# Kernel optimization log

Hardware: AMD Instinct MI355X
Metric: run time of the kernel (lower is better)

## Reference

```python
import jax, jax.numpy as jnp
import numpy as np

HIDDEN = 2048
NHEADS = 16
NKV = 4
HEAD_DIM = 128
B, T = 2, 2048


def setup_inputs() -> dict:
    key = jax.random.key(0)
    ks = jax.random.split(key, 7)
    x = jax.random.normal(ks[0], (B, T, HIDDEN), dtype=jnp.float32)
    # rope tables [T, head_dim//2]
    inv_freq = 1.0 / (10000.0 ** (jnp.arange(0, HEAD_DIM // 2, dtype=jnp.float32) / (HEAD_DIM // 2)))
    pos = jnp.arange(T, dtype=jnp.float32)
    ang = pos[:, None] * inv_freq[None, :]
    cos, sin = jnp.cos(ang), jnp.sin(ang)
    s = 0.02
    wq = jax.random.normal(ks[1], (HIDDEN, NHEADS * HEAD_DIM), dtype=jnp.float32) * s
    wk = jax.random.normal(ks[2], (HIDDEN, NKV * HEAD_DIM), dtype=jnp.float32) * s
    wv = jax.random.normal(ks[3], (HIDDEN, NKV * HEAD_DIM), dtype=jnp.float32) * s
    wo = jax.random.normal(ks[4], (NHEADS * HEAD_DIM, HIDDEN), dtype=jnp.float32) * s
    return {"x": x, "cos": cos, "sin": sin, "wq": wq, "wk": wk, "wv": wv, "wo": wo}


def _apply_rope(x, cos, sin):
    # x: [B, H, T, D]; cos/sin: [T, D//2]
    hd = x.shape[-1]
    x1, x2 = x[..., : hd // 2], x[..., hd // 2 :]
    c = cos[None, None, : x.shape[2], :]
    s = sin[None, None, : x.shape[2], :]
    return jnp.concatenate([x1 * c - x2 * s, x2 * c + x1 * s], axis=-1)


def reference(x, cos, sin, wq, wk, wv, wo):
    Bb, Tt, _ = x.shape
    q = (x @ wq).reshape(Bb, Tt, NHEADS, HEAD_DIM).transpose(0, 2, 1, 3)  # [B,H,T,D]
    k = (x @ wk).reshape(Bb, Tt, NKV, HEAD_DIM).transpose(0, 2, 1, 3)    # [B,Hk,T,D]
    v = (x @ wv).reshape(Bb, Tt, NKV, HEAD_DIM).transpose(0, 2, 1, 3)
    q = _apply_rope(q, cos, sin)
    k = _apply_rope(k, cos, sin)
    groups = NHEADS // NKV
    k = jnp.repeat(k, groups, axis=1)  # [B,H,T,D]
    v = jnp.repeat(v, groups, axis=1)
    scale = 1.0 / jnp.sqrt(jnp.asarray(HEAD_DIM, dtype=x.dtype))
    scores = jnp.einsum("bhqd,bhkd->bhqk", q, k) * scale
    causal = jnp.tril(jnp.ones((Tt, Tt), dtype=bool))
    scores = jnp.where(causal[None, None, :, :], scores, jnp.asarray(-jnp.inf, dtype=scores.dtype))
    attn = jax.nn.softmax(scores, axis=-1)
    out = jnp.einsum("bhqk,bhkd->bhqd", attn, v)
    out = out.transpose(0, 2, 1, 3).reshape(Bb, Tt, NHEADS * HEAD_DIM)
    return out @ wo
```

## Files before the change

kernel.cpp:

```cpp
#include <hip/hip_runtime.h>

#define HIDDEN 2048
#define NHEADS 16
#define NKV 4
#define HEAD_DIM 128
#define BB 2
#define TT 2048
#define MROWS (BB * TT)
#define NQKV (NHEADS * HEAD_DIM + 2 * NKV * HEAD_DIM)

typedef __attribute__((ext_vector_type(8))) short short8;
typedef __attribute__((ext_vector_type(4))) float f32x4;

#if __has_builtin(__builtin_amdgcn_exp2f)
#define EXP2F __builtin_amdgcn_exp2f
#else
#define EXP2F exp2f
#endif

__device__ __forceinline__ unsigned short f2bf(float f) {
    unsigned int u = __float_as_uint(f);
    unsigned int r = u + 0x7fffu + ((u >> 16) & 1u);
    return (unsigned short)(r >> 16);
}
__device__ __forceinline__ float b2f(unsigned short h) {
    return __uint_as_float(((unsigned int)h) << 16);
}

__device__ __forceinline__ void store_out(float* p, float v) { *p = v; }
__device__ __forceinline__ void store_out(unsigned short* p, float v) { *p = f2bf(v); }

__device__ __forceinline__ void load_lds_16(const void* g, void* l) {
    __builtin_amdgcn_global_load_lds((const __attribute__((address_space(1))) unsigned int*)g,
                                     (__attribute__((address_space(3))) unsigned int*)l,
                                     16, 0, 0);
}

__global__ void cast_x_kernel(const float* __restrict__ x, unsigned short* __restrict__ xb) {
    int i = blockIdx.x * 256 + threadIdx.x;
    float4 v = ((const float4*)x)[i];
    ushort4 o;
    o.x = f2bf(v.x); o.y = f2bf(v.y); o.z = f2bf(v.z); o.w = f2bf(v.w);
    ((ushort4*)xb)[i] = o;
}

__global__ void pack_wqkvT_kernel(const float* __restrict__ wq, const float* __restrict__ wk,
                                  const float* __restrict__ wv, unsigned short* __restrict__ out) {
    __shared__ float tile[32][33];
    int n0 = blockIdx.x * 32, k0 = blockIdx.y * 32;
    int tx = threadIdx.x, ty = threadIdx.y;
#pragma unroll
    for (int i = 0; i < 32; i += 8) {
        int k = k0 + ty + i;
        int n = n0 + tx;
        float v;
        if (n < 2048)      v = wq[(size_t)k * 2048 + n];
        else if (n < 2560) v = wk[(size_t)k * 512 + (n - 2048)];
        else               v = wv[(size_t)k * 512 + (n - 2560)];
        tile[ty + i][tx] = v;
    }
    __syncthreads();
#pragma unroll
    for (int i = 0; i < 32; i += 8) {
        int n = n0 + ty + i;
        int k = k0 + tx;
        out[(size_t)n * HIDDEN + k] = f2bf(tile[tx][ty + i]);
    }
}

__global__ void pack_woT_kernel(const float* __restrict__ wo, unsigned short* __restrict__ out) {
    __shared__ float tile[32][33];
    int n0 = blockIdx.x * 32, k0 = blockIdx.y * 32;
    int tx = threadIdx.x, ty = threadIdx.y;
#pragma unroll
    for (int i = 0; i < 32; i += 8)
        tile[ty + i][tx] = wo[(size_t)(k0 + ty + i) * HIDDEN + n0 + tx];
    __syncthreads();
#pragma unroll
    for (int i = 0; i < 32; i += 8)
        out[(size_t)(n0 + ty + i) * HIDDEN + k0 + tx] = f2bf(tile[tx][ty + i]);
}

template <typename OutT>
__global__ __launch_bounds__(512, 2) void gemm256_kernel(const unsigned short* __restrict__ A,
                                                         const unsigned short* __restrict__ Bt,
                                                         OutT* __restrict__ C,
                                                         int M, int N, int K, int NBX) {
    __shared__ __align__(16) unsigned short sbuf[2][2][256 * 64];
    const int tid = threadIdx.x;
    const int lane = tid & 63, w = tid >> 6;
    const int quad = lane >> 4, l15 = lane & 15;
    const int wrM = w >> 2, wcN = w & 3;

    const int nwg = gridDim.x;
    const int bswz = (blockIdx.x & 7) * (nwg >> 3) + (blockIdx.x >> 3);
    const int m0 = (bswz / NBX) * 256;
    const int n0 = (bswz % NBX) * 256;

    const int lr = tid >> 3;
    const int sc = (tid & 7) ^ (lr & 7);
    const unsigned short* gA = A + (size_t)(m0 + lr) * K + sc * 8;
    const unsigned short* gB = Bt + (size_t)(n0 + lr) * K + sc * 8;
    const size_t jstep = (size_t)64 * K;

    const int s0 = (quad ^ (l15 & 7)) * 8;
    const int s1 = ((4 | quad) ^ (l15 & 7)) * 8;

    f32x4 acc[8][4];
    const f32x4 z4 = {0.f, 0.f, 0.f, 0.f};
#pragma unroll
    for (int mi = 0; mi < 8; ++mi)
#pragma unroll
        for (int ni = 0; ni < 4; ++ni) acc[mi][ni] = z4;

#pragma unroll
    for (int j = 0; j < 4; ++j) {
        load_lds_16(gA + (size_t)j * jstep, &sbuf[0][0][j * 4096 + w * 512]);
        load_lds_16(gB + (size_t)j * jstep, &sbuf[0][1][j * 4096 + w * 512]);
    }
    __asm__ volatile("s_waitcnt vmcnt(0)" ::: "memory");
    __builtin_amdgcn_s_barrier();

    const int NT = K >> 6;
    for (int kt = 0; kt < NT; ++kt) {
        const int buf = kt & 1;
        const unsigned short* bA = &sbuf[buf][0][0];
        const unsigned short* bB = &sbuf[buf][1][0];

        if (kt + 1 < NT) {
            const size_t kof = (size_t)(kt + 1) * 64;
#pragma unroll
            for (int j = 0; j < 4; ++j) {
                load_lds_16(gA + (size_t)j * jstep + kof, &sbuf[buf ^ 1][0][j * 4096 + w * 512]);
                load_lds_16(gB + (size_t)j * jstep + kof, &sbuf[buf ^ 1][1][j * 4096 + w * 512]);
            }
        }

        short8 bf0[4], bf1[4];
#pragma unroll
        for (int ni = 0; ni < 4; ++ni) {
            const unsigned short* br = bB + (wcN * 64 + ni * 16 + l15) * 64;
            bf0[ni] = *(const short8*)(br + s0);
            bf1[ni] = *(const short8*)(br + s1);
        }

#pragma unroll
        for (int ph = 0; ph < 4; ++ph) {
            short8 af0[2], af1[2];
#pragma unroll
            for (int mm = 0; mm < 2; ++mm) {
                const unsigned short* ar = bA + (wrM * 128 + (ph * 2 + mm) * 16 + l15) * 64;
                af0[mm] = *(const short8*)(ar + s0);
                af1[mm] = *(const short8*)(ar + s1);
            }
            if (ph == 3 && kt + 1 < NT) {
                __asm__ volatile("s_waitcnt vmcnt(0)" ::: "memory");
            }
            __builtin_amdgcn_s_barrier();
            __asm__ volatile("s_waitcnt lgkmcnt(0)" ::: "memory");
            __builtin_amdgcn_s_setprio(1);
#pragma unroll
            for (int mm = 0; mm < 2; ++mm)
#pragma unroll
                for (int ni = 0; ni < 4; ++ni) {
                    acc[ph * 2 + mm][ni] =
                        __builtin_amdgcn_mfma_f32_16x16x32_bf16(af0[mm], bf0[ni], acc[ph * 2 + mm][ni], 0, 0, 0);
                    acc[ph * 2 + mm][ni] =
                        __builtin_amdgcn_mfma_f32_16x16x32_bf16(af1[mm], bf1[ni], acc[ph * 2 + mm][ni], 0, 0, 0);
                }
            __builtin_amdgcn_s_setprio(0);
            __builtin_amdgcn_s_barrier();
        }
    }

#pragma unroll
    for (int mi = 0; mi < 8; ++mi)
#pragma unroll
        for (int ni = 0; ni < 4; ++ni)
#pragma unroll
            for (int r = 0; r < 4; ++r) {
                int gr = m0 + wrM * 128 + mi * 16 + quad * 4 + r;
                int gc = n0 + wcN * 64 + ni * 16 + l15;
                store_out(&C[(size_t)gr * N + gc], acc[mi][ni][r]);
            }
}

#define QP (MROWS * NHEADS * 64)
#define KP (MROWS * NKV * 64)
#define QSCL (0.08838834764831845f * 1.4426950408889634f)
__global__ void rope_kernel(const unsigned short* __restrict__ qkv,
                            const float* __restrict__ cosb, const float* __restrict__ sinb,
                            unsigned short* __restrict__ Q, unsigned short* __restrict__ K) {
    int tid = blockIdx.x * 256 + threadIdx.x;
    if (tid < QP) {
        int d = tid & 63;
        int h = (tid >> 6) & 15;
        int row = tid >> 10;
        int t = row & (TT - 1), b = row >> 11;
        float x1 = b2f(qkv[(size_t)row * NQKV + h * 128 + d]);
        float x2 = b2f(qkv[(size_t)row * NQKV + h * 128 + d + 64]);
        float c = cosb[t * 64 + d], s = sinb[t * 64 + d];
        unsigned short* dst = Q + ((size_t)(b * NHEADS + h) * TT + t) * 128 + d;
        dst[0]  = f2bf((x1 * c - x2 * s) * QSCL);
        dst[64] = f2bf((x2 * c + x1 * s) * QSCL);
    } else {
        int p = tid - QP;
        int d = p & 63;
        int kh = (p >> 6) & 3;
        int row = p >> 8;
        int t = row & (TT - 1), b = row >> 11;
        float x1 = b2f(qkv[(size_t)row * NQKV + 2048 + kh * 128 + d]);
        float x2 = b2f(qkv[(size_t)row * NQKV + 2048 + kh * 128 + d + 64]);
        float c = cosb[t * 64 + d], s = sinb[t * 64 + d];
        unsigned short* dst = K + ((size_t)(b * NKV + kh) * TT + t) * 128 + d;
        dst[0]  = f2bf(x1 * c - x2 * s);
        dst[64] = f2bf(x2 * c + x1 * s);
    }
}

__global__ void vtrans_kernel(const unsigned short* __restrict__ qkv,
                              unsigned short* __restrict__ Vt) {
    __shared__ unsigned short tile[32][33];
    int t0 = blockIdx.x * 32, d0 = blockIdx.y * 32, bz = blockIdx.z;
    int b = bz >> 2, kh = bz & 3;
    int tx = threadIdx.x, ty = threadIdx.y;
#pragma unroll
    for (int i = 0; i < 32; i += 8)
        tile[ty + i][tx] = qkv[(size_t)(b * TT + t0 + ty + i) * NQKV + 2560 + kh * 128 + d0 + tx];
    __syncthreads();
#pragma unroll
    for (int i = 0; i < 32; i += 8)
        Vt[((size_t)bz * 128 + d0 + ty + i) * TT + t0 + tx] = tile[tx][ty + i];
}

#define PS 68
__global__ __launch_bounds__(256, 3) void flash_kernel(const unsigned short* __restrict__ Qb,
                                                       const unsigned short* __restrict__ Kb,
                                                       const unsigned short* __restrict__ Vtb,
                                                       unsigned short* __restrict__ Ob,
                                                       unsigned short* __restrict__ Po,
                                                       float* __restrict__ Pl) {
    __shared__ __align__(16) unsigned short sK[4][64 * 32];
    __shared__ __align__(16) unsigned short sV[2][128 * 32];
    __shared__ __align__(16) unsigned short sP[4][32 * PS];

    const int tid = threadIdx.x;
    const int w = tid >> 6, lane = tid & 63;
    const int quad = lane >> 4, l15 = lane & 15;

    const int lin = blockIdx.x;
    const int member = lin >> 8;
    const int rem = lin & 255;
    const int h = rem & 15;
    const int b = (rem >> 4) & 1;
    const int j = rem >> 5;
    int qb, kvlo, kvhi;
    bool partial;
    if (member == 2) {
        qb = j; kvlo = 0; kvhi = (qb + 1) * 128; partial = false;
    } else {
        qb = 15 - j;
        int half = (qb + 1) * 64;
        kvlo = member ? half : 0;
        kvhi = member ? (qb + 1) * 128 : half;
        partial = true;
    }
    const int q0 = qb * 128;
    const int kvh = h >> 2;
    const unsigned short* Qh = Qb + (size_t)(b * NHEADS + h) * TT * 128;
    const unsigned short* Kh = Kb + (size_t)(b * NKV + kvh) * TT * 128;
    const unsigned short* Vth = Vtb + (size_t)(b * NKV + kvh) * 128 * TT;

    const int wrow0 = q0 + w * 32;

    const unsigned short* gK = Kh + (size_t)(lane >> 2) * 128 + w * 32 + (lane & 3) * 8;
    const int vkf = w >> 1;
    const unsigned short* gV = Vth + (size_t)((w & 1) * 64 + (lane >> 2)) * TT + vkf * 32 + (lane & 3) * 8;

    short8 aq[2][4];
#pragma unroll
    for (int mi = 0; mi < 2; ++mi)
#pragma unroll
        for (int dk = 0; dk < 4; ++dk)
            aq[mi][dk] = *(const short8*)(Qh + (size_t)(wrow0 + mi * 16 + l15) * 128 + dk * 32 + quad * 8);

    f32x4 accO[2][8], accL[2];
    const f32x4 z4 = {0.f, 0.f, 0.f, 0.f};
#pragma unroll
    for (int mi = 0; mi < 2; ++mi) {
        accL[mi] = z4;
#pragma unroll
        for (int nb = 0; nb < 8; ++nb) accO[mi][nb] = z4;
    }

    const short kone = (short)0x3F80;
    const short8 ones = {kone, kone, kone, kone, kone, kone, kone, kone};
    unsigned short* sPw = &sP[w][0];

    for (int kv0 = kvlo; kv0 < kvhi; kv0 += 64) {
        __syncthreads();
#pragma unroll
        for (int g = 0; g < 4; ++g)
            load_lds_16(gK + (size_t)(kv0 + g * 16) * 128, &sK[w][g * 512]);
#pragma unroll
        for (int jj = 0; jj < 4; ++jj)
            load_lds_16(gV + kv0 + (size_t)(jj * 16) * TT, &sV[vkf][((w & 1) * 64 + jj * 16) * 32]);
        __syncthreads();

        if (kv0 <= wrow0 + 31) {
            f32x4 st[4][2];
#pragma unroll
            for (int t = 0; t < 4; ++t)
#pragma unroll
                for (int h2 = 0; h2 < 2; ++h2) st[t][h2] = z4;
#pragma unroll
            for (int t = 0; t < 4; ++t) {
#pragma unroll
                for (int dk = 0; dk < 4; ++dk) {
                    short8 ak = *(const short8*)(&sK[dk][(t * 16 + l15) * 32 + quad * 8]);
                    st[t][0] = __builtin_amdgcn_mfma_f32_16x16x32_bf16(ak, aq[0][dk], st[t][0], 0, 0, 0);
                    st[t][1] = __builtin_amdgcn_mfma_f32_16x16x32_bf16(ak, aq[1][dk], st[t][1], 0, 0, 0);
                }
            }
#pragma unroll
            for (int h2 = 0; h2 < 2; ++h2) {
                const int rowbase = (h2 * 16 + l15) * PS;
                const int qg = wrow0 + h2 * 16 + l15;
#pragma unroll
                for (int t = 0; t < 4; ++t) {
                    const int kvb = kv0 + t * 16 + quad * 4;
                    const bool nm = (kv0 + t * 16 + 15) > (wrow0 + h2 * 16);
                    union { unsigned short u[4]; uint2 v; } pk;
#pragma unroll
                    for (int r = 0; r < 4; ++r) {
                        float p = EXP2F(st[t][h2][r]);
                        if (nm) p = (kvb + r <= qg) ? p : 0.f;
                        pk.u[r] = f2bf(p);
                    }
                    *(uint2*)(&sPw[rowbase + t * 16 + quad * 4]) = pk.v;
                }
            }
            __asm__ volatile("s_waitcnt lgkmcnt(0)" ::: "memory");
            short8 ap[2][2];
#pragma unroll
            for (int mi = 0; mi < 2; ++mi) {
#pragma unroll
                for (int kf = 0; kf < 2; ++kf)
                    ap[mi][kf] = *(const short8*)(&sPw[(mi * 16 + l15) * PS + kf * 32 + quad * 8]);
                accL[mi] = __builtin_amdgcn_mfma_f32_16x16x32_bf16(ap[mi][0], ones, accL[mi], 0, 0, 0);
                accL[mi] = __builtin_amdgcn_mfma_f32_16x16x32_bf16(ap[mi][1], ones, accL[mi], 0, 0, 0);
            }
#pragma unroll
            for (int nb = 0; nb < 8; ++nb) {
                short8 bv0 = *(const short8*)(&sV[0][(nb * 16 + l15) * 32 + quad * 8]);
                short8 bv1 = *(const short8*)(&sV[1][(nb * 16 + l15) * 32 + quad * 8]);
#pragma unroll
                for (int mi = 0; mi < 2; ++mi) {
                    accO[mi][nb] = __builtin_amdgcn_mfma_f32_16x16x32_bf16(ap[mi][0], bv0, accO[mi][nb], 0, 0, 0);
                    accO[mi][nb] = __builtin_amdgcn_mfma_f32_16x16x32_bf16(ap[mi][1], bv1, accO[mi][nb], 0, 0, 0);
                }
            }
        }
    }

    if (!partial) {
        float inv[2][4];
#pragma unroll
        for (int mi = 0; mi < 2; ++mi)
#pragma unroll
            for (int r = 0; r < 4; ++r) inv[mi][r] = 1.0f / accL[mi][r];

        const size_t obase = ((size_t)b * TT + wrow0) * (NHEADS * HEAD_DIM) + h * 128;
#pragma unroll
        for (int half = 0; half < 2; ++half) {
            __asm__ volatile("s_waitcnt lgkmcnt(0)" ::: "memory");
#pragma unroll
            for (int mi = 0; mi < 2; ++mi)
#pragma unroll
                for (int nb2 = 0; nb2 < 4; ++nb2)
#pragma unroll
                    for (int r = 0; r < 4; ++r)
                        sPw[(mi * 16 + quad * 4 + r) * PS + nb2 * 16 + l15] =
                            f2bf(accO[mi][half * 4 + nb2][r] * inv[mi][r]);
            __asm__ volatile("s_waitcnt lgkmcnt(0)" ::: "memory");
#pragma unroll
            for (int pass = 0; pass < 4; ++pass) {
                int row2 = pass * 8 + (lane >> 3);
                short8 vv = *(const short8*)(&sPw[row2 * PS + (lane & 7) * 8]);
                *(short8*)(Ob + obase + (size_t)row2 * (NHEADS * HEAD_DIM) + half * 64 + (lane & 7) * 8) = vv;
            }
        }
    } else {
        const int part = member;
        const size_t pbase = ((size_t)(part * 2 + b) * 1024 + (wrow0 - 1024)) * 2048 + h * 128;
#pragma unroll
        for (int half = 0; half < 2; ++half) {
            __asm__ volatile("s_waitcnt lgkmcnt(0)" ::: "memory");
#pragma unroll
            for (int mi = 0; mi < 2; ++mi)
#pragma unroll
                for (int nb2 = 0; nb2 < 4; ++nb2)
#pragma unroll
                    for (int r = 0; r < 4; ++r)
                        sPw[(mi * 16 + quad * 4 + r) * PS + nb2 * 16 + l15] =
                            f2bf(accO[mi][half * 4 + nb2][r]);
            __asm__ volatile("s_waitcnt lgkmcnt(0)" ::: "memory");
#pragma unroll
            for (int pass = 0; pass < 4; ++pass) {
                int row2 = pass * 8 + (lane >> 3);
                short8 vv = *(const short8*)(&sPw[row2 * PS + (lane & 7) * 8]);
                *(short8*)(Po + pbase + (size_t)row2 * 2048 + half * 64 + (lane & 7) * 8) = vv;
            }
        }
        float* plb = Pl + ((size_t)(part * 2 + b) * 16 + h) * 1024 + (wrow0 - 1024);
        if (l15 == 0) {
#pragma unroll
            for (int mi = 0; mi < 2; ++mi)
#pragma unroll
                for (int r = 0; r < 4; ++r)
                    plb[mi * 16 + quad * 4 + r] = accL[mi][r];
        }
    }
}

__global__ void merge_kernel(const unsigned short* __restrict__ Po, const float* __restrict__ Pl,
                             unsigned short* __restrict__ attn) {
    int gid = blockIdx.x * 256 + threadIdx.x;
    size_t e8 = (size_t)gid * 8;
    int col = (int)(e8 & 2047);
    int rl  = (int)((e8 >> 11) & 1023);
    int b   = (int)(e8 >> 21);
    int h   = col >> 7;
    size_t i0 = ((size_t)b * 1024 + rl) * 2048 + col;
    size_t i1 = ((size_t)(2 + b) * 1024 + rl) * 2048 + col;
    float l = Pl[((size_t)b * 16 + h) * 1024 + rl] + Pl[((size_t)(2 + b) * 16 + h) * 1024 + rl];
    float inv = 1.0f / l;
    union { uint4 v; unsigned short u[8]; } a, c, o;
    a.v = *(const uint4*)(Po + i0);
    c.v = *(const uint4*)(Po + i1);
#pragma unroll
    for (int k = 0; k < 8; ++k)
        o.u[k] = f2bf((b2f(a.u[k]) + b2f(c.u[k])) * inv);
    *(uint4*)(attn + ((size_t)b * 2048 + 1024 + rl) * 2048 + col) = o.v;
}

extern "C" void kernel_launch(void* const* d_in, const int* in_sizes, int n_in,
                              void* d_out, int out_size, void* d_ws, size_t ws_size,
                              hipStream_t stream) {
    const float* x    = (const float*)d_in[0];
    const float* cosb = (const float*)d_in[1];
    const float* sinb = (const float*)d_in[2];
    const float* wq   = (const float*)d_in[3];
    const float* wk   = (const float*)d_in[4];
    const float* wv   = (const float*)d_in[5];
    const float* wo   = (const float*)d_in[6];
    float* out = (float*)d_out;

    char* ws = (char*)d_ws;
    unsigned short* xb    = (unsigned short*)(ws);
    unsigned short* wqkvT = (unsigned short*)(ws + (16u << 20));
    unsigned short* woT   = (unsigned short*)(ws + (28u << 20));
    unsigned short* qkv   = (unsigned short*)(ws + (36u << 20));
    unsigned short* Qbuf  = (unsigned short*)(ws + (60u << 20));
    unsigned short* Kbuf  = (unsigned short*)(ws + (76u << 20));
    unsigned short* Vt    = (unsigned short*)(ws + (80u << 20));
    unsigned short* attn  = (unsigned short*)(ws + (84u << 20));
    unsigned short* Po    = (unsigned short*)(ws);
    float*          Pl    = (float*)(ws + (16u << 20));

    cast_x_kernel<<<(MROWS * HIDDEN) / 4 / 256, 256, 0, stream>>>(x, xb);
    pack_wqkvT_kernel<<<dim3(NQKV / 32, HIDDEN / 32), dim3(32, 8), 0, stream>>>(wq, wk, wv, wqkvT);
    pack_woT_kernel<<<dim3(HIDDEN / 32, HIDDEN / 32), dim3(32, 8), 0, stream>>>(wo, woT);

    gemm256_kernel<unsigned short><<<dim3((MROWS / 256) * (NQKV / 256)), 512, 0, stream>>>(
        xb, wqkvT, qkv, MROWS, NQKV, HIDDEN, NQKV / 256);

    rope_kernel<<<(QP + KP) / 256, 256, 0, stream>>>(qkv, cosb, sinb, Qbuf, Kbuf);
    vtrans_kernel<<<dim3(TT / 32, HEAD_DIM / 32, BB * NKV), dim3(32, 8), 0, stream>>>(qkv, Vt);

    flash_kernel<<<dim3(768), 256, 0, stream>>>(Qbuf, Kbuf, Vt, attn, Po, Pl);
    merge_kernel<<<dim3(2048), 256, 0, stream>>>(Po, Pl, attn);

    gemm256_kernel<float><<<dim3((MROWS / 256) * (HIDDEN / 256)), 512, 0, stream>>>(
        attn, woT, out, MROWS, HIDDEN, HIDDEN, HIDDEN / 256);
}
```

Before: 340.3 us.

## Double-buffer K/V tiles in flash attention and drop split-KV merge

Rewrites the flash attention kernel to double-buffer K and V tiles in LDS, prefetching the next tile while the current one is computed. LDS layouts switch to XOR-swizzled rows in place of padding to avoid bank conflicts, and s_setprio is raised around the MFMA sections. The split-KV scheme for long query blocks and its merge kernel are removed, with each block now processing a full causal range. This reduces the grid to 512 blocks at 2 blocks/CU. The intent is to hide global load latency and drop the partial-output round trip, at the risk of load imbalance across the causal blocks and lower occupancy.

New measurement: 339.0 us. Within noise of the previous version (-0.4%).

```diff
diff --git a/kernel.cpp b/kernel.cpp
--- a/kernel.cpp
+++ b/kernel.cpp
@@ -233,39 +233,29 @@
         Vt[((size_t)bz * 128 + d0 + ty + i) * TT + t0 + tx] = tile[tx][ty + i];
 }
 
-#define PS 68
-__global__ __launch_bounds__(256, 3) void flash_kernel(const unsigned short* __restrict__ Qb,
+__global__ __launch_bounds__(256, 2) void flash_kernel(const unsigned short* __restrict__ Qb,
                                                        const unsigned short* __restrict__ Kb,
                                                        const unsigned short* __restrict__ Vtb,
-                                                       unsigned short* __restrict__ Ob,
-                                                       unsigned short* __restrict__ Po,
-                                                       float* __restrict__ Pl) {
-    __shared__ __align__(16) unsigned short sK[4][64 * 32];
-    __shared__ __align__(16) unsigned short sV[2][128 * 32];
-    __shared__ __align__(16) unsigned short sP[4][32 * PS];
+                                                       unsigned short* __restrict__ Ob) {
+    __shared__ __align__(16) unsigned short sK[2][64 * 128];
+    __shared__ __align__(16) unsigned short sV[2][128 * 64];
+    __shared__ __align__(16) unsigned short sP[4][32 * 64];
 
     const int tid = threadIdx.x;
     const int w = tid >> 6, lane = tid & 63;
     const int quad = lane >> 4, l15 = lane & 15;
+    const int r7 = l15 & 7;
 
     const int lin = blockIdx.x;
     const int member = lin >> 8;
-    const int rem = lin & 255;
-    const int h = rem & 15;
-    const int b = (rem >> 4) & 1;
-    const int j = rem >> 5;
-    int qb, kvlo, kvhi;
-    bool partial;
-    if (member == 2) {
-        qb = j; kvlo = 0; kvhi = (qb + 1) * 128; partial = false;
-    } else {
-        qb = 15 - j;
-        int half = (qb + 1) * 64;
-        kvlo = member ? half : 0;
-        kvhi = member ? (qb + 1) * 128 : half;
-        partial = true;
-    }
+    const int id = lin & 255;
+    const int h = id & 15;
+    const int b = (id >> 4) & 1;
+    const int j = id >> 5;
+    const int qb = member ? j : (15 - j);
     const int q0 = qb * 128;
+    const int ntile = (qb + 1) * 2;
+
     const int kvh = h >> 2;
     const unsigned short* Qh = Qb + (size_t)(b * NHEADS + h) * TT * 128;
     const unsigned short* Kh = Kb + (size_t)(b * NKV + kvh) * TT * 128;
@@ -273,9 +263,11 @@
 
     const int wrow0 = q0 + w * 32;
 
-    const unsigned short* gK = Kh + (size_t)(lane >> 2) * 128 + w * 32 + (lane & 3) * 8;
-    const int vkf = w >> 1;
-    const unsigned short* gV = Vth + (size_t)((w & 1) * 64 + (lane >> 2)) * TT + vkf * 32 + (lane & 3) * 8;
+    const int kr = lane >> 4;
+    const unsigned short* gKe = Kh + (size_t)(w * 16 + kr) * 128 + (((lane & 15) ^ kr) * 8);
+    const unsigned short* gKo = Kh + (size_t)(w * 16 + 4 + kr) * 128 + (((lane & 15) ^ (4 + kr)) * 8);
+    const int vr = lane >> 3;
+    const unsigned short* gV0 = Vth + (size_t)(w * 32 + vr) * TT + (((lane & 7) ^ vr) * 8);
 
     short8 aq[2][4];
 #pragma unroll
@@ -297,15 +289,33 @@
     const short8 ones = {kone, kone, kone, kone, kone, kone, kone, kone};
     unsigned short* sPw = &sP[w][0];
 
-    for (int kv0 = kvlo; kv0 < kvhi; kv0 += 64) {
-        __syncthreads();
-#pragma unroll
-        for (int g = 0; g < 4; ++g)
-            load_lds_16(gK + (size_t)(kv0 + g * 16) * 128, &sK[w][g * 512]);
-#pragma unroll
-        for (int jj = 0; jj < 4; ++jj)
-            load_lds_16(gV + kv0 + (size_t)(jj * 16) * TT, &sV[vkf][((w & 1) * 64 + jj * 16) * 32]);
-        __syncthreads();
+#pragma unroll
+    for (int g = 0; g < 4; ++g) {
+        const unsigned short* src = (g & 1) ? gKo : gKe;
+        load_lds_16(src + (size_t)(g >> 1) * 8 * 128, &sK[0][(w * 4 + g) * 512]);
+    }
+#pragma unroll
+    for (int g = 0; g < 4; ++g)
+        load_lds_16(gV0 + (size_t)(g * 8) * TT, &sV[0][(w * 4 + g) * 512]);
+
+    for (int it = 0; it < ntile; ++it) {
+        const int cur = it & 1;
+        const int kv0 = it * 64;
+        if (it + 1 < ntile) {
+            const size_t kvn = (size_t)(it + 1) * 64;
+#pragma unroll
+            for (int g = 0; g < 4; ++g) {
+                const unsigned short* src = (g & 1) ? gKo : gKe;
+                load_lds_16(src + (kvn + (size_t)(g >> 1) * 8) * 128, &sK[cur ^ 1][(w * 4 + g) * 512]);
+            }
+#pragma unroll
+            for (int g = 0; g < 4; ++g)
+                load_lds_16(gV0 + (size_t)(g * 8) * TT + kvn, &sV[cur ^ 1][(w * 4 + g) * 512]);
+            __asm__ volatile("s_waitcnt vmcnt(8)" ::: "memory");
+        } else {
+            __asm__ volatile("s_waitcnt vmcnt(0)" ::: "memory");
+        }
+        __builtin_amdgcn_s_barrier();
 
         if (kv0 <= wrow0 + 31) {
             f32x4 st[4][2];
@@ -313,18 +323,20 @@
             for (int t = 0; t < 4; ++t)
 #pragma unroll
                 for (int h2 = 0; h2 < 2; ++h2) st[t][h2] = z4;
+            __builtin_amdgcn_s_setprio(1);
 #pragma unroll
             for (int t = 0; t < 4; ++t) {
 #pragma unroll
                 for (int dk = 0; dk < 4; ++dk) {
-                    short8 ak = *(const short8*)(&sK[dk][(t * 16 + l15) * 32 + quad * 8]);
+                    short8 ak = *(const short8*)(&sK[cur][(t * 16 + l15) * 128 + ((dk * 4 + quad) ^ r7) * 8]);
                     st[t][0] = __builtin_amdgcn_mfma_f32_16x16x32_bf16(ak, aq[0][dk], st[t][0], 0, 0, 0);
                     st[t][1] = __builtin_amdgcn_mfma_f32_16x16x32_bf16(ak, aq[1][dk], st[t][1], 0, 0, 0);
                 }
             }
+            __builtin_amdgcn_s_setprio(0);
 #pragma unroll
             for (int h2 = 0; h2 < 2; ++h2) {
-                const int rowbase = (h2 * 16 + l15) * PS;
+                const int rowbase = (h2 * 16 + l15) * 64;
                 const int qg = wrow0 + h2 * 16 + l15;
 #pragma unroll
                 for (int t = 0; t < 4; ++t) {
@@ -337,7 +349,7 @@
                         if (nm) p = (kvb + r <= qg) ? p : 0.f;
                         pk.u[r] = f2bf(p);
                     }
-                    *(uint2*)(&sPw[rowbase + t * 16 + quad * 4]) = pk.v;
+                    *(uint2*)(&sPw[rowbase + (((2 * t + (quad >> 1)) ^ r7) * 8) + (quad & 1) * 4]) = pk.v;
                 }
             }
             __asm__ volatile("s_waitcnt lgkmcnt(0)" ::: "memory");
@@ -346,102 +358,54 @@
             for (int mi = 0; mi < 2; ++mi) {
 #pragma unroll
                 for (int kf = 0; kf < 2; ++kf)
-                    ap[mi][kf] = *(const short8*)(&sPw[(mi * 16 + l15) * PS + kf * 32 + quad * 8]);
+                    ap[mi][kf] = *(const short8*)(&sPw[(mi * 16 + l15) * 64 + ((kf * 4 + quad) ^ r7) * 8]);
                 accL[mi] = __builtin_amdgcn_mfma_f32_16x16x32_bf16(ap[mi][0], ones, accL[mi], 0, 0, 0);
                 accL[mi] = __builtin_amdgcn_mfma_f32_16x16x32_bf16(ap[mi][1], ones, accL[mi], 0, 0, 0);
             }
+            __builtin_amdgcn_s_setprio(1);
 #pragma unroll
             for (int nb = 0; nb < 8; ++nb) {
-                short8 bv0 = *(const short8*)(&sV[0][(nb * 16 + l15) * 32 + quad * 8]);
-                short8 bv1 = *(const short8*)(&sV[1][(nb * 16 + l15) * 32 + quad * 8]);
+                short8 bv0 = *(const short8*)(&sV[cur][(nb * 16 + l15) * 64 + ((quad) ^ r7) * 8]);
+                short8 bv1 = *(const short8*)(&sV[cur][(nb * 16 + l15) * 64 + ((4 + quad) ^ r7) * 8]);
 #pragma unroll
                 for (int mi = 0; mi < 2; ++mi) {
                     accO[mi][nb] = __builtin_amdgcn_mfma_f32_16x16x32_bf16(ap[mi][0], bv0, accO[mi][nb], 0, 0, 0);
                     accO[mi][nb] = __builtin_amdgcn_mfma_f32_16x16x32_bf16(ap[mi][1], bv1, accO[mi][nb], 0, 0, 0);
                 }
             }
-        }
-    }
-
-    if (!partial) {
-        float inv[2][4];
+            __builtin_amdgcn_s_setprio(0);
+        }
+        __builtin_amdgcn_s_barrier();
+    }
+
+    float inv[2][4];
+#pragma unroll
+    for (int mi = 0; mi < 2; ++mi)
+#pragma unroll
+        for (int r = 0; r < 4; ++r) inv[mi][r] = 1.0f / accL[mi][r];
+
+    const size_t obase = ((size_t)b * TT + wrow0) * (NHEADS * HEAD_DIM) + h * 128;
+#pragma unroll
+    for (int half = 0; half < 2; ++half) {
+        __asm__ volatile("s_waitcnt lgkmcnt(0)" ::: "memory");
 #pragma unroll
         for (int mi = 0; mi < 2; ++mi)
 #pragma unroll
-            for (int r = 0; r < 4; ++r) inv[mi][r] = 1.0f / accL[mi][r];
-
-        const size_t obase = ((size_t)b * TT + wrow0) * (NHEADS * HEAD_DIM) + h * 128;
-#pragma unroll
-        for (int half = 0; half < 2; ++half) {
-            __asm__ volatile("s_waitcnt lgkmcnt(0)" ::: "memory");
-#pragma unroll
-            for (int mi = 0; mi < 2; ++mi)
-#pragma unroll
-                for (int nb2 = 0; nb2 < 4; ++nb2)
-#pragma unroll
-                    for (int r = 0; r < 4; ++r)
-                        sPw[(mi * 16 + quad * 4 + r) * PS + nb2 * 16 + l15] =
-                            f2bf(accO[mi][half * 4 + nb2][r] * inv[mi][r]);
-            __asm__ volatile("s_waitcnt lgkmcnt(0)" ::: "memory");
-#pragma unroll
-            for (int pass = 0; pass < 4; ++pass) {
-                int row2 = pass * 8 + (lane >> 3);
-                short8 vv = *(const short8*)(&sPw[row2 * PS + (lane & 7) * 8]);
-                *(short8*)(Ob + obase + (size_t)row2 * (NHEADS * HEAD_DIM) + half * 64 + (lane & 7) * 8) = vv;
-            }
-        }
-    } else {
-        const int part = member;
-        const size_t pbase = ((size_t)(part * 2 + b) * 1024 + (wrow0 - 1024)) * 2048 + h * 128;
-#pragma unroll
-        for (int half = 0; half < 2; ++half) {
-            __asm__ volatile("s_waitcnt lgkmcnt(0)" ::: "memory");
-#pragma unroll
-            for (int mi = 0; mi < 2; ++mi)
-#pragma unroll
-                for (int nb2 = 0; nb2 < 4; ++nb2)
-#pragma unroll
-                    for (int r = 0; r < 4; ++r)
-                        sPw[(mi * 16 + quad * 4 + r) * PS + nb2 * 16 + l15] =
-                            f2bf(accO[mi][half * 4 + nb2][r]);
-            __asm__ volatile("s_waitcnt lgkmcnt(0)" ::: "memory");
-#pragma unroll
-            for (int pass = 0; pass < 4; ++pass) {
-                int row2 = pass * 8 + (lane >> 3);
-                short8 vv = *(const short8*)(&sPw[row2 * PS + (lane & 7) * 8]);
-                *(short8*)(Po + pbase + (size_t)row2 * 2048 + half * 64 + (lane & 7) * 8) = vv;
-            }
-        }
-        float* plb = Pl + ((size_t)(part * 2 + b) * 16 + h) * 1024 + (wrow0 - 1024);
-        if (l15 == 0) {
-#pragma unroll
-            for (int mi = 0; mi < 2; ++mi)
-#pragma unroll
-                for (int r = 0; r < 4; ++r)
-                    plb[mi * 16 + quad * 4 + r] = accL[mi][r];
-        }
-    }
-}
-
-__global__ void merge_kernel(const unsigned short* __restrict__ Po, const float* __restrict__ Pl,
-                             unsigned short* __restrict__ attn) {
-    int gid = blockIdx.x * 256 + threadIdx.x;
-    size_t e8 = (size_t)gid * 8;
-    int col = (int)(e8 & 2047);
-    int rl  = (int)((e8 >> 11) & 1023);
-    int b   = (int)(e8 >> 21);
-    int h   = col >> 7;
-    size_t i0 = ((size_t)b * 1024 + rl) * 2048 + col;
-    size_t i1 = ((size_t)(2 + b) * 1024 + rl) * 2048 + col;
-    float l = Pl[((size_t)b * 16 + h) * 1024 + rl] + Pl[((size_t)(2 + b) * 16 + h) * 1024 + rl];
-    float inv = 1.0f / l;
-    union { uint4 v; unsigned short u[8]; } a, c, o;
-    a.v = *(const uint4*)(Po + i0);
-    c.v = *(const uint4*)(Po + i1);
-#pragma unroll
-    for (int k = 0; k < 8; ++k)
-        o.u[k] = f2bf((b2f(a.u[k]) + b2f(c.u[k])) * inv);
-    *(uint4*)(attn + ((size_t)b * 2048 + 1024 + rl) * 2048 + col) = o.v;
+            for (int nb2 = 0; nb2 < 4; ++nb2)
+#pragma unroll
+                for (int r = 0; r < 4; ++r) {
+                    const int row = mi * 16 + quad * 4 + r;
+                    sPw[row * 64 + (((2 * nb2 + (l15 >> 3)) ^ (row & 7)) * 8) + r7] =
+                        f2bf(accO[mi][half * 4 + nb2][r] * inv[mi][r]);
+                }
+        __asm__ volatile("s_waitcnt lgkmcnt(0)" ::: "memory");
+#pragma unroll
+        for (int pass = 0; pass < 4; ++pass) {
+            int row2 = pass * 8 + (lane >> 3);
+            short8 vv = *(const short8*)(&sPw[row2 * 64 + (((lane & 7) ^ (row2 & 7)) * 8)]);
+            *(short8*)(Ob + obase + (size_t)row2 * (NHEADS * HEAD_DIM) + half * 64 + (lane & 7) * 8) = vv;
+        }
+    }
 }
 
 extern "C" void kernel_launch(void* const* d_in, const int* in_sizes, int n_in,
@@ -465,8 +429,6 @@
     unsigned short* Kbuf  = (unsigned short*)(ws + (76u << 20));
     unsigned short* Vt    = (unsigned short*)(ws + (80u << 20));
     unsigned short* attn  = (unsigned short*)(ws + (84u << 20));
-    unsigned short* Po    = (unsigned short*)(ws);
-    float*          Pl    = (float*)(ws + (16u << 20));
 
     cast_x_kernel<<<(MROWS * HIDDEN) / 4 / 256, 256, 0, stream>>>(x, xb);
     pack_wqkvT_kernel<<<dim3(NQKV / 32, HIDDEN / 32), dim3(32, 8), 0, stream>>>(wq, wk, wv, wqkvT);
@@ -478,8 +440,7 @@
     rope_kernel<<<(QP + KP) / 256, 256, 0, stream>>>(qkv, cosb, sinb, Qbuf, Kbuf);
     vtrans_kernel<<<dim3(TT / 32, HEAD_DIM / 32, BB * NKV), dim3(32, 8), 0, stream>>>(qkv, Vt);
 
-    flash_kernel<<<dim3(768), 256, 0, stream>>>(Qbuf, Kbuf, Vt, attn, Po, Pl);
-    merge_kernel<<<dim3(2048), 256, 0, stream>>>(Po, Pl, attn);
+    flash_kernel<<<dim3(512), 256, 0, stream>>>(Qbuf, Kbuf, Vt, attn);
 
     gemm256_kernel<float><<<dim3((MROWS / 256) * (HIDDEN / 256)), 512, 0, stream>>>(
         attn, woT, out, MROWS, HIDDEN, HIDDEN, HIDDEN / 256);
```

## Double-buffer K in flash attention, keep P in registers, add narrower output GEMM

Applied to the files above, without the earlier changes.

Restructures the flash attention loop so the next K tile is prefetched into a second LDS buffer while the current tile computes. The loads use XOR-swizzled LDS layouts to avoid bank conflicts. The P matrix is now converted with packed bf16 instructions and moved between lanes with shuffles instead of a round trip through LDS. The row sum is accumulated in scalar registers rather than by an MFMA against a ones vector. The output projection also switches to a new 256x128-tile GEMM, which doubles the number of workgroups to improve occupancy and wave balance, at the cost of more shuffle ALU work and extra A-tile reloads.

Result: faster. 318.8 us (-6.3%).

```diff
diff --git a/kernel.cpp b/kernel.cpp
--- a/kernel.cpp
+++ b/kernel.cpp
@@ -182,6 +182,107 @@
                 int gr = m0 + wrM * 128 + mi * 16 + quad * 4 + r;
                 int gc = n0 + wcN * 64 + ni * 16 + l15;
                 store_out(&C[(size_t)gr * N + gc], acc[mi][ni][r]);
+            }
+}
+
+__global__ __launch_bounds__(512, 2) void gemm256n128_kernel(const unsigned short* __restrict__ A,
+                                                             const unsigned short* __restrict__ Bt,
+                                                             float* __restrict__ C,
+                                                             int M, int N, int K, int NBX) {
+    __shared__ __align__(16) unsigned short sA[2][256 * 64];
+    __shared__ __align__(16) unsigned short sB[2][128 * 64];
+    const int tid = threadIdx.x;
+    const int lane = tid & 63, w = tid >> 6;
+    const int quad = lane >> 4, l15 = lane & 15;
+    const int wrM = w >> 1, wcN = w & 1;
+
+    const int nwg = gridDim.x;
+    const int bswz = (blockIdx.x & 7) * (nwg >> 3) + (blockIdx.x >> 3);
+    const int m0 = (bswz / NBX) * 256;
+    const int n0 = (bswz % NBX) * 128;
+
+    const int lr = tid >> 3;
+    const int sc = (tid & 7) ^ (lr & 7);
+    const unsigned short* gA = A + (size_t)(m0 + lr) * K + sc * 8;
+    const unsigned short* gB = Bt + (size_t)(n0 + lr) * K + sc * 8;
+    const size_t jstep = (size_t)64 * K;
+
+    const int s0 = (quad ^ (l15 & 7)) * 8;
+    const int s1 = ((4 | quad) ^ (l15 & 7)) * 8;
+
+    f32x4 acc[4][4];
+    const f32x4 z4 = {0.f, 0.f, 0.f, 0.f};
+#pragma unroll
+    for (int mi = 0; mi < 4; ++mi)
+#pragma unroll
+        for (int ni = 0; ni < 4; ++ni) acc[mi][ni] = z4;
+
+#pragma unroll
+    for (int j = 0; j < 4; ++j)
+        load_lds_16(gA + (size_t)j * jstep, &sA[0][j * 4096 + w * 512]);
+#pragma unroll
+    for (int j = 0; j < 2; ++j)
+        load_lds_16(gB + (size_t)j * jstep, &sB[0][j * 4096 + w * 512]);
+    __asm__ volatile("s_waitcnt vmcnt(0)" ::: "memory");
+    __builtin_amdgcn_s_barrier();
+
+    const int NT = K >> 6;
+    for (int kt = 0; kt < NT; ++kt) {
+        const int buf = kt & 1;
+        const unsigned short* bA = &sA[buf][0];
+        const unsigned short* bB = &sB[buf][0];
+
+        if (kt + 1 < NT) {
+            const size_t kof = (size_t)(kt + 1) * 64;
+#pragma unroll
+            for (int j = 0; j < 4; ++j)
+                load_lds_16(gA + (size_t)j * jstep + kof, &sA[buf ^ 1][j * 4096 + w * 512]);
+#pragma unroll
+            for (int j = 0; j < 2; ++j)
+                load_lds_16(gB + (size_t)j * jstep + kof, &sB[buf ^ 1][j * 4096 + w * 512]);
+        }
+
+        short8 bf0[4], bf1[4];
+#pragma unroll
+        for (int ni = 0; ni < 4; ++ni) {
+            const unsigned short* br = bB + (wcN * 64 + ni * 16 + l15) * 64;
+            bf0[ni] = *(const short8*)(br + s0);
+            bf1[ni] = *(const short8*)(br + s1);
+        }
+
+#pragma unroll
+        for (int ph = 0; ph < 4; ++ph) {
+            short8 af0, af1;
+            {
+                const unsigned short* ar = bA + (wrM * 64 + ph * 16 + l15) * 64;
+                af0 = *(const short8*)(ar + s0);
+                af1 = *(const short8*)(ar + s1);
+            }
+            if (ph == 3 && kt + 1 < NT) {
+                __asm__ volatile("s_waitcnt vmcnt(0)" ::: "memory");
+            }
+            __builtin_amdgcn_s_barrier();
+            __asm__ volatile("s_waitcnt lgkmcnt(0)" ::: "memory");
+            __builtin_amdgcn_s_setprio(1);
+#pragma unroll
+            for (int ni = 0; ni < 4; ++ni) {
+                acc[ph][ni] = __builtin_amdgcn_mfma_f32_16x16x32_bf16(af0, bf0[ni], acc[ph][ni], 0, 0, 0);
+                acc[ph][ni] = __builtin_amdgcn_mfma_f32_16x16x32_bf16(af1, bf1[ni], acc[ph][ni], 0, 0, 0);
+            }
+            __builtin_amdgcn_s_setprio(0);
+            __builtin_amdgcn_s_barrier();
+        }
+    }
+
+#pragma unroll
+    for (int mi = 0; mi < 4; ++mi)
+#pragma unroll
+        for (int ni = 0; ni < 4; ++ni)
+#pragma unroll
+            for (int r = 0; r < 4; ++r) {
+                int gr = m0 + wrM * 64 + mi * 16 + quad * 4 + r;
+                int gc = n0 + wcN * 64 + ni * 16 + l15;
+                C[(size_t)gr * N + gc] = acc[mi][ni][r];
             }
 }
 
@@ -233,20 +334,19 @@
         Vt[((size_t)bz * 128 + d0 + ty + i) * TT + t0 + tx] = tile[tx][ty + i];
 }
 
-#define PS 68
 __global__ __launch_bounds__(256, 3) void flash_kernel(const unsigned short* __restrict__ Qb,
                                                        const unsigned short* __restrict__ Kb,
                                                        const unsigned short* __restrict__ Vtb,
                                                        unsigned short* __restrict__ Ob,
                                                        unsigned short* __restrict__ Po,
                                                        float* __restrict__ Pl) {
-    __shared__ __align__(16) unsigned short sK[4][64 * 32];
-    __shared__ __align__(16) unsigned short sV[2][128 * 32];
-    __shared__ __align__(16) unsigned short sP[4][32 * PS];
+    __shared__ __align__(16) unsigned short sK[2][64 * 128];
+    __shared__ __align__(16) unsigned short sV[128 * 64];
 
     const int tid = threadIdx.x;
     const int w = tid >> 6, lane = tid & 63;
     const int quad = lane >> 4, l15 = lane & 15;
+    const int r7 = l15 & 7;
 
     const int lin = blockIdx.x;
     const int member = lin >> 8;
@@ -266,6 +366,7 @@
         partial = true;
     }
     const int q0 = qb * 128;
+    const int ntile = (kvhi - kvlo) >> 6;
     const int kvh = h >> 2;
     const unsigned short* Qh = Qb + (size_t)(b * NHEADS + h) * TT * 128;
     const unsigned short* Kh = Kb + (size_t)(b * NKV + kvh) * TT * 128;
@@ -273,9 +374,11 @@
 
     const int wrow0 = q0 + w * 32;
 
-    const unsigned short* gK = Kh + (size_t)(lane >> 2) * 128 + w * 32 + (lane & 3) * 8;
-    const int vkf = w >> 1;
-    const unsigned short* gV = Vth + (size_t)((w & 1) * 64 + (lane >> 2)) * TT + vkf * 32 + (lane & 3) * 8;
+    const int kr = lane >> 4;
+    const unsigned short* gKe = Kh + (size_t)(w * 16 + kr) * 128 + (((lane & 15) ^ kr) * 8);
+    const unsigned short* gKo = Kh + (size_t)(w * 16 + 4 + kr) * 128 + (((lane & 15) ^ (4 + kr)) * 8);
+    const int vr = lane >> 3;
+    const unsigned short* gV0 = Vth + (size_t)(w * 32 + vr) * TT + (((lane & 7) ^ vr) * 8);
 
     short8 aq[2][4];
 #pragma unroll
@@ -284,92 +387,129 @@
         for (int dk = 0; dk < 4; ++dk)
             aq[mi][dk] = *(const short8*)(Qh + (size_t)(wrow0 + mi * 16 + l15) * 128 + dk * 32 + quad * 8);
 
-    f32x4 accO[2][8], accL[2];
+    f32x4 accO[2][8];
+    float accLc[2] = {0.f, 0.f};
     const f32x4 z4 = {0.f, 0.f, 0.f, 0.f};
 #pragma unroll
-    for (int mi = 0; mi < 2; ++mi) {
-        accL[mi] = z4;
+    for (int mi = 0; mi < 2; ++mi)
 #pragma unroll
         for (int nb = 0; nb < 8; ++nb) accO[mi][nb] = z4;
-    }
-
-    const short kone = (short)0x3F80;
-    const short8 ones = {kone, kone, kone, kone, kone, kone, kone, kone};
-    unsigned short* sPw = &sP[w][0];
-
-    for (int kv0 = kvlo; kv0 < kvhi; kv0 += 64) {
-        __syncthreads();
+
+#pragma unroll
+    for (int g = 0; g < 4; ++g) {
+        const unsigned short* src = (g & 1) ? gKo : gKe;
+        load_lds_16(src + (size_t)(kvlo + (g >> 1) * 8) * 128, &sK[0][(w * 4 + g) * 512]);
+    }
+
+    for (int it = 0; it < ntile; ++it) {
+        const int cur = it & 1;
+        const int kv0 = kvlo + it * 64;
+        __asm__ volatile("s_waitcnt vmcnt(0)" ::: "memory");
+        __builtin_amdgcn_s_barrier();
 #pragma unroll
         for (int g = 0; g < 4; ++g)
-            load_lds_16(gK + (size_t)(kv0 + g * 16) * 128, &sK[w][g * 512]);
-#pragma unroll
-        for (int jj = 0; jj < 4; ++jj)
-            load_lds_16(gV + kv0 + (size_t)(jj * 16) * TT, &sV[vkf][((w & 1) * 64 + jj * 16) * 32]);
-        __syncthreads();
-
-        if (kv0 <= wrow0 + 31) {
+            load_lds_16(gV0 + (size_t)(g * 8) * TT + kv0, &sV[(w * 4 + g) * 512]);
+        const bool hasn = (it + 1 < ntile);
+        if (hasn) {
+#pragma unroll
+            for (int g = 0; g < 4; ++g) {
+                const unsigned short* src = (g & 1) ? gKo : gKe;
+                load_lds_16(src + (size_t)(kv0 + 64 + (g >> 1) * 8) * 128, &sK[cur ^ 1][(w * 4 + g) * 512]);
+            }
+        }
+        const bool compute = (kv0 <= wrow0 + 31);
+        short8 ap[2][2];
+        if (compute) {
             f32x4 st[4][2];
 #pragma unroll
             for (int t = 0; t < 4; ++t)
 #pragma unroll
                 for (int h2 = 0; h2 < 2; ++h2) st[t][h2] = z4;
+            __builtin_amdgcn_s_setprio(1);
 #pragma unroll
             for (int t = 0; t < 4; ++t) {
 #pragma unroll
                 for (int dk = 0; dk < 4; ++dk) {
-                    short8 ak = *(const short8*)(&sK[dk][(t * 16 + l15) * 32 + quad * 8]);
+                    short8 ak = *(const short8*)(&sK[cur][(t * 16 + l15) * 128 + ((dk * 4 + quad) ^ r7) * 8]);
                     st[t][0] = __builtin_amdgcn_mfma_f32_16x16x32_bf16(ak, aq[0][dk], st[t][0], 0, 0, 0);
                     st[t][1] = __builtin_amdgcn_mfma_f32_16x16x32_bf16(ak, aq[1][dk], st[t][1], 0, 0, 0);
                 }
             }
+            __builtin_amdgcn_s_setprio(0);
+            unsigned int pk32[4][2][2];
 #pragma unroll
             for (int h2 = 0; h2 < 2; ++h2) {
-                const int rowbase = (h2 * 16 + l15) * PS;
                 const int qg = wrow0 + h2 * 16 + l15;
 #pragma unroll
                 for (int t = 0; t < 4; ++t) {
                     const int kvb = kv0 + t * 16 + quad * 4;
                     const bool nm = (kv0 + t * 16 + 15) > (wrow0 + h2 * 16);
-                    union { unsigned short u[4]; uint2 v; } pk;
+                    float pv[4];
 #pragma unroll
                     for (int r = 0; r < 4; ++r) {
                         float p = EXP2F(st[t][h2][r]);
                         if (nm) p = (kvb + r <= qg) ? p : 0.f;
-                        pk.u[r] = f2bf(p);
+                        pv[r] = p;
                     }
-                    *(uint2*)(&sPw[rowbase + t * 16 + quad * 4]) = pk.v;
+                    accLc[h2] += (pv[0] + pv[1]) + (pv[2] + pv[3]);
+                    __asm__("v_cvt_pk_bf16_f32 %0, %1, %2" : "=v"(pk32[t][h2][0]) : "v"(pv[0]), "v"(pv[1]));
+                    __asm__("v_cvt_pk_bf16_f32 %0, %1, %2" : "=v"(pk32[t][h2][1]) : "v"(pv[2]), "v"(pv[3]));
                 }
             }
-            __asm__ volatile("s_waitcnt lgkmcnt(0)" ::: "memory");
-            short8 ap[2][2];
-#pragma unroll
-            for (int mi = 0; mi < 2; ++mi) {
-#pragma unroll
-                for (int kf = 0; kf < 2; ++kf)
-                    ap[mi][kf] = *(const short8*)(&sPw[(mi * 16 + l15) * PS + kf * 32 + quad * 8]);
-                accL[mi] = __builtin_amdgcn_mfma_f32_16x16x32_bf16(ap[mi][0], ones, accL[mi], 0, 0, 0);
-                accL[mi] = __builtin_amdgcn_mfma_f32_16x16x32_bf16(ap[mi][1], ones, accL[mi], 0, 0, 0);
-            }
+#pragma unroll
+            for (int h2 = 0; h2 < 2; ++h2)
+#pragma unroll
+                for (int kf = 0; kf < 2; ++kf) {
+                    union { unsigned int u[4]; short8 s8; } W;
+#pragma unroll
+                    for (int wdx = 0; wdx < 4; ++wdx) {
+                        int srcl = (2 * (quad & 1) + (wdx >> 1)) * 16 + l15;
+                        unsigned int a0 = (unsigned int)__shfl((int)pk32[2 * kf][h2][wdx & 1], srcl, 64);
+                        unsigned int a1 = (unsigned int)__shfl((int)pk32[2 * kf + 1][h2][wdx & 1], srcl, 64);
+                        W.u[wdx] = (quad >> 1) ? a1 : a0;
+                    }
+                    ap[h2][kf] = W.s8;
+                }
+        }
+        if (hasn) { __asm__ volatile("s_waitcnt vmcnt(4)" ::: "memory"); }
+        else      { __asm__ volatile("s_waitcnt vmcnt(0)" ::: "memory"); }
+        __builtin_amdgcn_s_barrier();
+        if (compute) {
+            __builtin_amdgcn_s_setprio(1);
 #pragma unroll
             for (int nb = 0; nb < 8; ++nb) {
-                short8 bv0 = *(const short8*)(&sV[0][(nb * 16 + l15) * 32 + quad * 8]);
-                short8 bv1 = *(const short8*)(&sV[1][(nb * 16 + l15) * 32 + quad * 8]);
+                short8 bv0 = *(const short8*)(&sV[(nb * 16 + l15) * 64 + ((quad) ^ r7) * 8]);
+                short8 bv1 = *(const short8*)(&sV[(nb * 16 + l15) * 64 + ((4 + quad) ^ r7) * 8]);
 #pragma unroll
                 for (int mi = 0; mi < 2; ++mi) {
                     accO[mi][nb] = __builtin_amdgcn_mfma_f32_16x16x32_bf16(ap[mi][0], bv0, accO[mi][nb], 0, 0, 0);
                     accO[mi][nb] = __builtin_amdgcn_mfma_f32_16x16x32_bf16(ap[mi][1], bv1, accO[mi][nb], 0, 0, 0);
                 }
             }
-        }
-    }
+            __builtin_amdgcn_s_setprio(0);
+        }
+    }
+
+    float Lr[2][4];
+#pragma unroll
+    for (int mi = 0; mi < 2; ++mi) {
+        float v = accLc[mi];
+        v += __shfl_xor(v, 16, 64);
+        v += __shfl_xor(v, 32, 64);
+#pragma unroll
+        for (int r = 0; r < 4; ++r)
+            Lr[mi][r] = __shfl(v, quad * 4 + r, 64);
+    }
+
+    __syncthreads();
+    unsigned short* sPw = &sV[w * 2048];
 
     if (!partial) {
         float inv[2][4];
 #pragma unroll
         for (int mi = 0; mi < 2; ++mi)
 #pragma unroll
-            for (int r = 0; r < 4; ++r) inv[mi][r] = 1.0f / accL[mi][r];
-
+            for (int r = 0; r < 4; ++r) inv[mi][r] = 1.0f / Lr[mi][r];
         const size_t obase = ((size_t)b * TT + wrow0) * (NHEADS * HEAD_DIM) + h * 128;
 #pragma unroll
         for (int half = 0; half < 2; ++half) {
@@ -379,20 +519,21 @@
 #pragma unroll
                 for (int nb2 = 0; nb2 < 4; ++nb2)
 #pragma unroll
-                    for (int r = 0; r < 4; ++r)
-                        sPw[(mi * 16 + quad * 4 + r) * PS + nb2 * 16 + l15] =
+                    for (int r = 0; r < 4; ++r) {
+                        const int row = mi * 16 + quad * 4 + r;
+                        sPw[row * 64 + (((2 * nb2 + (l15 >> 3)) ^ (row & 7)) * 8) + r7] =
                             f2bf(accO[mi][half * 4 + nb2][r] * inv[mi][r]);
+                    }
             __asm__ volatile("s_waitcnt lgkmcnt(0)" ::: "memory");
 #pragma unroll
             for (int pass = 0; pass < 4; ++pass) {
                 int row2 = pass * 8 + (lane >> 3);
-                short8 vv = *(const short8*)(&sPw[row2 * PS + (lane & 7) * 8]);
+                short8 vv = *(const short8*)(&sPw[row2 * 64 + (((lane & 7) ^ (row2 & 7)) * 8)]);
                 *(short8*)(Ob + obase + (size_t)row2 * (NHEADS * HEAD_DIM) + half * 64 + (lane & 7) * 8) = vv;
             }
         }
     } else {
-        const int part = member;
-        const size_t pbase = ((size_t)(part * 2 + b) * 1024 + (wrow0 - 1024)) * 2048 + h * 128;
+        const size_t pbase = ((size_t)(member * 2 + b) * 1024 + (wrow0 - 1024)) * 2048 + h * 128;
 #pragma unroll
         for (int half = 0; half < 2; ++half) {
             __asm__ volatile("s_waitcnt lgkmcnt(0)" ::: "memory");
@@ -401,24 +542,26 @@
 #pragma unroll
                 for (int nb2 = 0; nb2 < 4; ++nb2)
 #pragma unroll
-                    for (int r = 0; r < 4; ++r)
-                        sPw[(mi * 16 + quad * 4 + r) * PS + nb2 * 16 + l15] =
+                    for (int r = 0; r < 4; ++r) {
+                        const int row = mi * 16 + quad * 4 + r;
+                        sPw[row * 64 + (((2 * nb2 + (l15 >> 3)) ^ (row & 7)) * 8) + r7] =
                             f2bf(accO[mi][half * 4 + nb2][r]);
+                    }
             __asm__ volatile("s_waitcnt lgkmcnt(0)" ::: "memory");
 #pragma unroll
             for (int pass = 0; pass < 4; ++pass) {
                 int row2 = pass * 8 + (lane >> 3);
-                short8 vv = *(const short8*)(&sPw[row2 * PS + (lane & 7) * 8]);
+                short8 vv = *(const short8*)(&sPw[row2 * 64 + (((lane & 7) ^ (row2 & 7)) * 8)]);
                 *(short8*)(Po + pbase + (size_t)row2 * 2048 + half * 64 + (lane & 7) * 8) = vv;
             }
         }
-        float* plb = Pl + ((size_t)(part * 2 + b) * 16 + h) * 1024 + (wrow0 - 1024);
+        float* plb = Pl + ((size_t)(member * 2 + b) * 16 + h) * 1024 + (wrow0 - 1024);
         if (l15 == 0) {
 #pragma unroll
             for (int mi = 0; mi < 2; ++mi)
 #pragma unroll
                 for (int r = 0; r < 4; ++r)
-                    plb[mi * 16 + quad * 4 + r] = accL[mi][r];
+                    plb[mi * 16 + quad * 4 + r] = Lr[mi][r];
         }
     }
 }
@@ -481,6 +624,6 @@
     flash_kernel<<<dim3(768), 256, 0, stream>>>(Qbuf, Kbuf, Vt, attn, Po, Pl);
     merge_kernel<<<dim3(2048), 256, 0, stream>>>(Po, Pl, attn);
 
-    gemm256_kernel<float><<<dim3((MROWS / 256) * (HIDDEN / 256)), 512, 0, stream>>>(
-        attn, woT, out, MROWS, HIDDEN, HIDDEN, HIDDEN / 256);
-}
+    gemm256n128_kernel<<<dim3((MROWS / 256) * (HIDDEN / 128)), 512, 0, stream>>>(
+        attn, woT, out, MROWS, HIDDEN, HIDDEN, HIDDEN / 128);
+}
```
